# Kernel optimization log

Hardware: AMD Instinct MI355X
Metric: run time of the kernel (lower is better)

## Reference

```python
import math
import jax, jax.numpy as jnp
import numpy as np

B, N, D = 8, 1024, 1024
H, TKQ, TV = 16, 64, 64
DOUT = H * TV  # 1024, equals D
EPS = 1e-5


def _layer_norm(x, g, b):
    mu = jnp.mean(x, axis=-1, keepdims=True)
    var = jnp.mean((x - mu) ** 2, axis=-1, keepdims=True)
    return (x - mu) * jax.lax.rsqrt(var + EPS) * g + b


def setup_inputs() -> dict:
    key = jax.random.key(0)
    ks = jax.random.split(key, 16)
    s_w = 1.0 / math.sqrt(D)
    inp = {
        "tokens": jax.random.normal(ks[0], (B, N, D), jnp.float32),
        "Wq": jax.random.normal(ks[1], (H, D, TKQ), jnp.float32) * s_w,
        "bq": jax.random.uniform(ks[2], (H, 1, TKQ), jnp.float32, -s_w, s_w),
        "Wk": jax.random.normal(ks[3], (H, D, TKQ), jnp.float32) * s_w,
        "bk": jax.random.uniform(ks[4], (H, 1, TKQ), jnp.float32, -s_w, s_w),
        "Wv": jax.random.normal(ks[5], (H, D, TV), jnp.float32) * s_w,
        "bv": jax.random.uniform(ks[6], (H, 1, TV), jnp.float32, -s_w, s_w),
        "W1": jax.random.normal(ks[7], (DOUT, DOUT), jnp.float32) * (1.0 / math.sqrt(DOUT)),
        "b1": jax.random.uniform(ks[8], (DOUT,), jnp.float32, -s_w, s_w),
        "W2": jax.random.normal(ks[9], (DOUT, DOUT), jnp.float32) * (1.0 / math.sqrt(DOUT)),
        "b2": jax.random.uniform(ks[10], (DOUT,), jnp.float32, -s_w, s_w),
        "g1": jnp.ones((DOUT,), jnp.float32),
        "be1": jnp.zeros((DOUT,), jnp.float32),
        "g2": jnp.ones((DOUT,), jnp.float32),
        "be2": jnp.zeros((DOUT,), jnp.float32),
    }
    return inp


def reference(tokens, Wq, bq, Wk, bk, Wv, bv, W1, b1, W2, b2, g1, be1, g2, be2):
    # per-head projections: tokens[:,None] @ W + b  -> [B,H,N,T]
    tq = jnp.einsum("bnd,hdt->bhnt", tokens, Wq) + bq
    tk = jnp.einsum("bnd,hdt->bhnt", tokens, Wk) + bk
    tv = jnp.einsum("bnd,hdt->bhnt", tokens, Wv) + bv
    # non-standard scale: sqrt(num_heads * dim_tv)
    scale = math.sqrt(H * TV)
    scores = jnp.einsum("bhqt,bhkt->bhqk", tq, tk) / scale
    attn = jax.nn.softmax(scores, axis=-1)
    out = jnp.einsum("bhqk,bhkt->bhqt", attn, tv)  # [B,H,N,TV]
    # original flatten order: (B,N,TV,H) -> reshape(B,N,TV*H)
    out = jnp.transpose(out, (0, 2, 3, 1)).reshape(B, N, TV * H)
    # post-LN SAB path
    h = out + tokens
    h = _layer_norm(h, g1, be1)
    ff = jax.nn.relu(h @ W1 + b1) @ W2 + b2
    h = h + ff
    return _layer_norm(h, g2, be2)
```

## Files before the change

kernel.cpp:

```cpp
#include <hip/hip_runtime.h>
#include <hip/hip_bf16.h>

#define BB 8
#define NN_ 1024
#define DD 1024
#define HH 16
#define TT_ 64
#define MM (BB * NN_)

typedef __attribute__((ext_vector_type(8))) short short8;
typedef __attribute__((ext_vector_type(4))) float f32x4;
typedef __attribute__((ext_vector_type(4))) unsigned int u32x4;

__device__ __forceinline__ void g2lds16(const void* g, void* l) {
    __builtin_amdgcn_global_load_lds(
        (const __attribute__((address_space(1))) void*)g,
        (__attribute__((address_space(3))) void*)l, 16, 0, 0);
}

__device__ __forceinline__ __hip_bfloat16 f2b(float x) { return __float2bfloat16(x); }
__device__ __forceinline__ float b2f(unsigned short u) {
    unsigned v = (unsigned)u << 16;
    return __builtin_bit_cast(float, v);
}

__device__ __forceinline__ unsigned cvtpk(float a, float b) {
    unsigned r;
    asm("v_cvt_pk_bf16_f32 %0, %1, %2" : "=v"(r) : "v"(a), "v"(b));
    return r;
}

__global__ __launch_bounds__(256) void k_cvt_tokens(const float* __restrict__ in,
                                                    __hip_bfloat16* __restrict__ out) {
    int i = (blockIdx.x * 256 + threadIdx.x) * 4;
    float4 v = *(const float4*)&in[i];
    out[i + 0] = f2b(v.x); out[i + 1] = f2b(v.y);
    out[i + 2] = f2b(v.z); out[i + 3] = f2b(v.w);
}

__global__ __launch_bounds__(256) void k_cvt_wqkv(const float* __restrict__ Wq,
                                                  const float* __restrict__ Wk,
                                                  const float* __restrict__ Wv,
                                                  __hip_bfloat16* __restrict__ out) {
    __shared__ float tile[64][65];
    const int bid = blockIdx.x;
    const int proj = bid >> 8, h = (bid >> 4) & 15, dt = bid & 15;
    const float* W = proj == 0 ? Wq : (proj == 1 ? Wk : Wv);
    const float* src = W + ((size_t)h * 1024 + dt * 64) * 64;
    const int c = threadIdx.x & 63, r0 = threadIdx.x >> 6;
#pragma unroll
    for (int p = 0; p < 16; p++) {
        const int r = p * 4 + r0;
        tile[r][c] = src[(size_t)r * 64 + c];
    }
    __syncthreads();
    __hip_bfloat16* dst = out + (size_t)(proj * 1024 + h * 64) * 1024 + dt * 64;
#pragma unroll
    for (int p = 0; p < 16; p++) {
        const int r = p * 4 + r0;
        dst[(size_t)r * 1024 + c] = f2b(tile[c][r]);
    }
}

__global__ __launch_bounds__(256) void k_cvt_w(const float* __restrict__ W,
                                               __hip_bfloat16* __restrict__ out) {
    __shared__ float tile[64][65];
    const int ct = blockIdx.x & 15, dt = blockIdx.x >> 4;
    const float* src = W + (size_t)(dt * 64) * 1024 + ct * 64;
    const int c = threadIdx.x & 63, r0 = threadIdx.x >> 6;
#pragma unroll
    for (int p = 0; p < 16; p++) {
        const int r = p * 4 + r0;
        tile[r][c] = src[(size_t)r * 1024 + c];
    }
    __syncthreads();
    __hip_bfloat16* dst = out + (size_t)(ct * 64) * 1024 + dt * 64;
#pragma unroll
    for (int p = 0; p < 16; p++) {
        const int r = p * 4 + r0;
        dst[(size_t)r * 1024 + c] = f2b(tile[c][r]);
    }
}

template <int MODE>
__global__ __launch_bounds__(256) void k_gemm(
    const __hip_bfloat16* __restrict__ A, const __hip_bfloat16* __restrict__ Bt,
    const float* __restrict__ bias0, const float* __restrict__ bias1,
    const float* __restrict__ bias2,
    __hip_bfloat16* __restrict__ ob0, __hip_bfloat16* __restrict__ ob1,
    __hip_bfloat16* __restrict__ ob2,
    const __hip_bfloat16* __restrict__ res) {
    __shared__ __align__(16) __hip_bfloat16 As[128 * 64];
    __shared__ __align__(16) __hip_bfloat16 Bs[128 * 64];

    const int tid = threadIdx.x;
    const int wid = tid >> 6, lane = tid & 63;
    const int l15 = lane & 15, lhi = lane >> 4;
    const int wm = wid >> 1, wn = wid & 1;
    const int m0 = blockIdx.y * 128, n0 = blockIdx.x * 128;
    const int srow = lane >> 3, scol = (lane & 7) * 8;

    const __hip_bfloat16* gsrc;
    __hip_bfloat16* lbase;
    if (wid < 2) {
        gsrc = A + (size_t)(m0 + wid * 64 + srow) * 1024 + scol;
        lbase = As + wid * 64 * 64;
    } else {
        gsrc = Bt + (size_t)(n0 + (wid - 2) * 64 + srow) * 1024 + scol;
        lbase = Bs + (wid - 2) * 64 * 64;
    }

    f32x4 acc[4][4];
#pragma unroll
    for (int i = 0; i < 4; i++)
#pragma unroll
        for (int j = 0; j < 4; j++) acc[i][j] = (f32x4){0.f, 0.f, 0.f, 0.f};

    for (int kt = 0; kt < 16; ++kt) {
#pragma unroll
        for (int i = 0; i < 8; ++i)
            g2lds16(gsrc + kt * 64 + (size_t)i * 8 * 1024, lbase + i * 512);
        __syncthreads();
#pragma unroll
        for (int kk = 0; kk < 2; ++kk) {
            const int kb = kk * 32 + lhi * 8;
            short8 af[4], bfr[4];
#pragma unroll
            for (int mi = 0; mi < 4; mi++)
                af[mi] = *(const short8*)&As[(wm * 64 + mi * 16 + l15) * 64 + kb];
#pragma unroll
            for (int ni = 0; ni < 4; ni++)
                bfr[ni] = *(const short8*)&Bs[(wn * 64 + ni * 16 + l15) * 64 + kb];
#pragma unroll
            for (int mi = 0; mi < 4; mi++)
#pragma unroll
                for (int ni = 0; ni < 4; ni++)
                    acc[mi][ni] = __builtin_amdgcn_mfma_f32_16x16x32_bf16(
                        af[mi], bfr[ni], acc[mi][ni], 0, 0, 0);
        }
        __syncthreads();
    }

#pragma unroll
    for (int mi = 0; mi < 4; mi++) {
#pragma unroll
        for (int ni = 0; ni < 4; ni++) {
            const int col = n0 + wn * 64 + ni * 16 + l15;
#pragma unroll
            for (int r = 0; r < 4; r++) {
                const int m = m0 + wm * 64 + mi * 16 + lhi * 4 + r;
                float v = acc[mi][ni][r];
                if (MODE == 0) {
                    const int proj = col >> 10, hh = (col >> 6) & 15, t = col & 63;
                    const float* bp = proj == 0 ? bias0 : (proj == 1 ? bias1 : bias2);
                    v += bp[hh * 64 + t];
                    const int b = m >> 10, n = m & 1023;
                    if (proj == 0)
                        ob0[((size_t)(b * 16 + hh) * 1024 + n) * 64 + t] = f2b(v * 0.04508422f);
                    else if (proj == 1)
                        ob1[((size_t)(b * 16 + hh) * 1024 + n) * 64 + t] = f2b(v);
                    else
                        ob2[((size_t)(b * 16 + hh) * 64 + t) * 1024 + n] = f2b(v);
                } else if (MODE == 1) {
                    v += bias0[col];
                    ob0[(size_t)m * 1024 + col] = f2b(fmaxf(v, 0.f));
                } else {
                    v += bias0[col] + b2f(*(const unsigned short*)&res[(size_t)m * 1024 + col]);
                    ob0[(size_t)m * 1024 + col] = f2b(v);
                }
            }
        }
    }
}

__global__ __launch_bounds__(256) void k_attn(const __hip_bfloat16* __restrict__ Q,
                                              const __hip_bfloat16* __restrict__ Kg,
                                              const __hip_bfloat16* __restrict__ Vt,
                                              __hip_bfloat16* __restrict__ attn_out) {
    __shared__ __align__(16) __hip_bfloat16 Ks[2][64 * 64];
    __shared__ __align__(16) __hip_bfloat16 Vs[2][64 * 64];

    const int tid = threadIdx.x, wid = tid >> 6, lane = tid & 63;
    const int l15 = lane & 15, lhi = lane >> 4;
    const int bid = blockIdx.x;
    const int qb = bid & 7, head = (bid >> 3) & 15, b = bid >> 7;
    const int bh = b * 16 + head;
    const __hip_bfloat16* Qg = Q + ((size_t)bh * 1024 + qb * 128) * 64;
    const __hip_bfloat16* Kp = Kg + (size_t)bh * 1024 * 64;
    const __hip_bfloat16* Vp = Vt + (size_t)bh * 64 * 1024;
    const int srow = lane >> 3;
    const int scol = ((lane & 7) ^ srow) * 8;

    auto stageKV = [&](int t, int bufi) {
#pragma unroll
        for (int i = 0; i < 2; i++) {
            const int krow = (wid * 2 + i) * 8 + srow;
            const int kperm = (krow & 0x23) | ((krow & 0x0C) << 1) | ((krow & 0x10) >> 2);
            g2lds16(Kp + (size_t)(t * 64 + kperm) * 64 + scol, &Ks[bufi][(wid * 2 + i) * 512]);
            g2lds16(Vp + (size_t)krow * 1024 + t * 64 + scol, &Vs[bufi][(wid * 2 + i) * 512]);
        }
    };
    stageKV(0, 0);

    short8 qf[2][2];
#pragma unroll
    for (int g = 0; g < 2; g++)
#pragma unroll
        for (int c = 0; c < 2; c++)
            qf[g][c] = *(const short8*)&Qg[(size_t)(wid * 32 + g * 16 + l15) * 64 + c * 32 + lhi * 8];

    f32x4 o[2][4];
#pragma unroll
    for (int g = 0; g < 2; g++)
#pragma unroll
        for (int i = 0; i < 4; i++) o[g][i] = (f32x4){0.f, 0.f, 0.f, 0.f};
    f32x4 lacc[2] = {(f32x4){0.f, 0.f, 0.f, 0.f}, (f32x4){0.f, 0.f, 0.f, 0.f}};
    const short bf16_one = (short)0x3F80;
    const short8 ones = (short8){bf16_one, bf16_one, bf16_one, bf16_one,
                                 bf16_one, bf16_one, bf16_one, bf16_one};

    const int sw = l15 & 7;
    const int c0 = (lhi ^ sw) * 8;

    for (int t = 0; t < 16; ++t) {
        const int cur = t & 1;
        if (t < 15) {
            stageKV(t + 1, cur ^ 1);
            asm volatile("s_waitcnt vmcnt(4)" ::: "memory");
        } else {
            asm volatile("s_waitcnt vmcnt(0)" ::: "memory");
        }
        __builtin_amdgcn_s_barrier();
        asm volatile("" ::: "memory");

        f32x4 s[2][4];
        __builtin_amdgcn_s_setprio(1);
#pragma unroll
        for (int nt = 0; nt < 4; ++nt) {
            const int kr = (nt * 16 + l15) * 64;
            short8 k0 = *(const short8*)&Ks[cur][kr + c0];
            short8 k1 = *(const short8*)&Ks[cur][kr + (c0 ^ 32)];
#pragma unroll
            for (int g = 0; g < 2; g++) {
                f32x4 z = (f32x4){0.f, 0.f, 0.f, 0.f};
                z = __builtin_amdgcn_mfma_f32_16x16x32_bf16(k0, qf[g][0], z, 0, 0, 0);
                s[g][nt] = __builtin_amdgcn_mfma_f32_16x16x32_bf16(k1, qf[g][1], z, 0, 0, 0);
            }
        }
        __builtin_amdgcn_s_setprio(0);

#pragma unroll
        for (int g = 0; g < 2; g++)
#pragma unroll
            for (int nt = 0; nt < 4; nt++)
#pragma unroll
                for (int r = 0; r < 4; r++) s[g][nt][r] = __builtin_exp2f(s[g][nt][r]);

        short8 pf[2][2];
#pragma unroll
        for (int g = 0; g < 2; g++) {
            u32x4 w0 = (u32x4){cvtpk(s[g][0][0], s[g][0][1]), cvtpk(s[g][0][2], s[g][0][3]),
                               cvtpk(s[g][1][0], s[g][1][1]), cvtpk(s[g][1][2], s[g][1][3])};
            u32x4 w1 = (u32x4){cvtpk(s[g][2][0], s[g][2][1]), cvtpk(s[g][2][2], s[g][2][3]),
                               cvtpk(s[g][3][0], s[g][3][1]), cvtpk(s[g][3][2], s[g][3][3])};
            pf[g][0] = __builtin_bit_cast(short8, w0);
            pf[g][1] = __builtin_bit_cast(short8, w1);
        }

        __builtin_amdgcn_s_setprio(1);
#pragma unroll
        for (int g = 0; g < 2; g++) {
            lacc[g] = __builtin_amdgcn_mfma_f32_16x16x32_bf16(pf[g][0], ones, lacc[g], 0, 0, 0);
            lacc[g] = __builtin_amdgcn_mfma_f32_16x16x32_bf16(pf[g][1], ones, lacc[g], 0, 0, 0);
        }
#pragma unroll
        for (int tt = 0; tt < 4; tt++) {
            const int vr = (tt * 16 + l15) * 64;
            short8 v0 = *(const short8*)&Vs[cur][vr + c0];
            short8 v1 = *(const short8*)&Vs[cur][vr + (c0 ^ 32)];
#pragma unroll
            for (int g = 0; g < 2; g++) {
                o[g][tt] = __builtin_amdgcn_mfma_f32_16x16x32_bf16(pf[g][0], v0, o[g][tt], 0, 0, 0);
                o[g][tt] = __builtin_amdgcn_mfma_f32_16x16x32_bf16(pf[g][1], v1, o[g][tt], 0, 0, 0);
            }
        }
        __builtin_amdgcn_s_setprio(0);
        asm volatile("" ::: "memory");
        __builtin_amdgcn_s_barrier();
    }

#pragma unroll
    for (int g = 0; g < 2; g++)
#pragma unroll
        for (int r = 0; r < 4; r++) {
            const float inv_r = 1.f / lacc[g][r];
            const int row = qb * 128 + wid * 32 + g * 16 + lhi * 4 + r;
#pragma unroll
            for (int tt = 0; tt < 4; tt++) {
                const int ch = (tt * 16 + l15) * 16 + head;
                attn_out[((size_t)(b * 1024 + row)) * 1024 + ch] = f2b(o[g][tt][r] * inv_r);
            }
        }
}

__global__ __launch_bounds__(256) void k_ln1(const __hip_bfloat16* __restrict__ x1,
                                             const float* __restrict__ x2,
                                             const float* __restrict__ g,
                                             const float* __restrict__ be,
                                             __hip_bfloat16* __restrict__ y) {
    const int row = blockIdx.x;
    const int tid = threadIdx.x, wid = tid >> 6, lane = tid & 63;
    const int c = tid * 4;
    const ushort4 u = *(const ushort4*)&x1[(size_t)row * 1024 + c];
    float4 xv;
    xv.x = b2f(u.x); xv.y = b2f(u.y); xv.z = b2f(u.z); xv.w = b2f(u.w);
    float4 a = *(const float4*)&x2[(size_t)row * 1024 + c];
    xv.x += a.x; xv.y += a.y; xv.z += a.z; xv.w += a.w;
    float s = xv.x + xv.y + xv.z + xv.w;
    float q = xv.x * xv.x + xv.y * xv.y + xv.z * xv.z + xv.w * xv.w;
#pragma unroll
    for (int msk = 1; msk < 64; msk <<= 1) {
        s += __shfl_xor(s, msk);
        q += __shfl_xor(q, msk);
    }
    __shared__ float ss[4], qq[4];
    if (lane == 0) { ss[wid] = s; qq[wid] = q; }
    __syncthreads();
    s = ss[0] + ss[1] + ss[2] + ss[3];
    q = qq[0] + qq[1] + qq[2] + qq[3];
    const float mu = s * (1.f / 1024.f);
    const float var = q * (1.f / 1024.f) - mu * mu;
    const float rs = rsqrtf(var + 1e-5f);
    float4 gv = *(const float4*)&g[c];
    float4 bv = *(const float4*)&be[c];
    __hip_bfloat16* d = y + (size_t)row * 1024 + c;
    d[0] = f2b((xv.x - mu) * rs * gv.x + bv.x);
    d[1] = f2b((xv.y - mu) * rs * gv.y + bv.y);
    d[2] = f2b((xv.z - mu) * rs * gv.z + bv.z);
    d[3] = f2b((xv.w - mu) * rs * gv.w + bv.w);
}

__global__ __launch_bounds__(256) void k_ln2(const __hip_bfloat16* __restrict__ x,
                                             const float* __restrict__ g,
                                             const float* __restrict__ be,
                                             float* __restrict__ y) {
    const int row = blockIdx.x;
    const int tid = threadIdx.x, wid = tid >> 6, lane = tid & 63;
    const int c = tid * 4;
    const ushort4 u = *(const ushort4*)&x[(size_t)row * 1024 + c];
    float4 xv;
    xv.x = b2f(u.x); xv.y = b2f(u.y); xv.z = b2f(u.z); xv.w = b2f(u.w);
    float s = xv.x + xv.y + xv.z + xv.w;
    float q = xv.x * xv.x + xv.y * xv.y + xv.z * xv.z + xv.w * xv.w;
#pragma unroll
    for (int msk = 1; msk < 64; msk <<= 1) {
        s += __shfl_xor(s, msk);
        q += __shfl_xor(q, msk);
    }
    __shared__ float ss[4], qq[4];
    if (lane == 0) { ss[wid] = s; qq[wid] = q; }
    __syncthreads();
    s = ss[0] + ss[1] + ss[2] + ss[3];
    q = qq[0] + qq[1] + qq[2] + qq[3];
    const float mu = s * (1.f / 1024.f);
    const float var = q * (1.f / 1024.f) - mu * mu;
    const float rs = rsqrtf(var + 1e-5f);
    float4 gv = *(const float4*)&g[c];
    float4 bv = *(const float4*)&be[c];
    float4 yv;
    yv.x = (xv.x - mu) * rs * gv.x + bv.x;
    yv.y = (xv.y - mu) * rs * gv.y + bv.y;
    yv.z = (xv.z - mu) * rs * gv.z + bv.z;
    yv.w = (xv.w - mu) * rs * gv.w + bv.w;
    *(float4*)&y[(size_t)row * 1024 + c] = yv;
}

extern "C" void kernel_launch(void* const* d_in, const int* in_sizes, int n_in,
                              void* d_out, int out_size, void* d_ws, size_t ws_size,
                              hipStream_t stream) {
    const float* tokens = (const float*)d_in[0];
    const float* Wq  = (const float*)d_in[1];
    const float* bq  = (const float*)d_in[2];
    const float* Wk  = (const float*)d_in[3];
    const float* bk  = (const float*)d_in[4];
    const float* Wv  = (const float*)d_in[5];
    const float* bv  = (const float*)d_in[6];
    const float* W1  = (const float*)d_in[7];
    const float* b1  = (const float*)d_in[8];
    const float* W2  = (const float*)d_in[9];
    const float* b2  = (const float*)d_in[10];
    const float* g1  = (const float*)d_in[11];
    const float* be1 = (const float*)d_in[12];
    const float* g2  = (const float*)d_in[13];
    const float* be2 = (const float*)d_in[14];

    char* ws = (char*)d_ws;
    const size_t MB = 1024 * 1024;
    __hip_bfloat16* tok_b  = (__hip_bfloat16*)(ws + 0);
    __hip_bfloat16* Wqkv_t = (__hip_bfloat16*)(ws + 16 * MB);
    __hip_bfloat16* W1t    = (__hip_bfloat16*)(ws + 22 * MB);
    __hip_bfloat16* W2t    = (__hip_bfloat16*)(ws + 24 * MB);
    __hip_bfloat16* Qb     = (__hip_bfloat16*)(ws + 26 * MB);
    __hip_bfloat16* Kb     = (__hip_bfloat16*)(ws + 42 * MB);
    __hip_bfloat16* Vtb    = (__hip_bfloat16*)(ws + 58 * MB);
    __hip_bfloat16* attn_b = (__hip_bfloat16*)(ws + 74 * MB);
    __hip_bfloat16* h1     = (__hip_bfloat16*)(ws + 90 * MB);
    __hip_bfloat16* t1     = (__hip_bfloat16*)(ws + 26 * MB);
    __hip_bfloat16* h2     = (__hip_bfloat16*)(ws + 42 * MB);

    k_cvt_tokens<<<8192, 256, 0, stream>>>(tokens, tok_b);
    k_cvt_wqkv<<<768, 256, 0, stream>>>(Wq, Wk, Wv, Wqkv_t);
    k_cvt_w<<<256, 256, 0, stream>>>(W1, W1t);
    k_cvt_w<<<256, 256, 0, stream>>>(W2, W2t);

    k_gemm<0><<<dim3(24, 64), 256, 0, stream>>>(tok_b, Wqkv_t, bq, bk, bv,
                                                Qb, Kb, Vtb, nullptr);
    k_attn<<<1024, 256, 0, stream>>>(Qb, Kb, Vtb, attn_b);
    k_ln1<<<8192, 256, 0, stream>>>(attn_b, tokens, g1, be1, h1);
    k_gemm<1><<<dim3(8, 64), 256, 0, stream>>>(h1, W1t, b1, nullptr, nullptr,
                                               t1, nullptr, nullptr, nullptr);
    k_gemm<2><<<dim3(8, 64), 256, 0, stream>>>(t1, W2t, b2, nullptr, nullptr,
                                               h2, nullptr, nullptr, h1);
    k_ln2<<<8192, 256, 0, stream>>>(h2, g2, be2, (float*)d_out);
}
```

Before: 267.3 us.

## Double-buffer GEMM LDS tiles with XOR swizzle and prefetch overlap

The GEMM kernel now keeps two LDS buffers for the A and B tiles and issues the global-to-LDS loads for the next K tile before computing on the current one, using explicit vmcnt waits and raw barriers. The global source column is XOR-swizzled by row, so LDS fragment reads spread across banks instead of conflicting. s_setprio raises wave priority around the MFMA section. The goal is to hide global load latency and remove LDS bank conflicts. The cost is doubled LDS use (64KB), which may lower occupancy, and the correctness of the vmcnt accounting is delicate.

```diff
diff --git a/kernel.cpp b/kernel.cpp
--- a/kernel.cpp
+++ b/kernel.cpp
@@ -90,25 +90,30 @@
     __hip_bfloat16* __restrict__ ob0, __hip_bfloat16* __restrict__ ob1,
     __hip_bfloat16* __restrict__ ob2,
     const __hip_bfloat16* __restrict__ res) {
-    __shared__ __align__(16) __hip_bfloat16 As[128 * 64];
-    __shared__ __align__(16) __hip_bfloat16 Bs[128 * 64];
+    __shared__ __align__(16) __hip_bfloat16 As[2][128 * 64];
+    __shared__ __align__(16) __hip_bfloat16 Bs[2][128 * 64];
 
     const int tid = threadIdx.x;
     const int wid = tid >> 6, lane = tid & 63;
     const int l15 = lane & 15, lhi = lane >> 4;
     const int wm = wid >> 1, wn = wid & 1;
     const int m0 = blockIdx.y * 128, n0 = blockIdx.x * 128;
-    const int srow = lane >> 3, scol = (lane & 7) * 8;
+    const int srow = lane >> 3;
+    const int scol = ((lane & 7) ^ srow) * 8;
 
     const __hip_bfloat16* gsrc;
-    __hip_bfloat16* lbase;
-    if (wid < 2) {
+    if (wid < 2)
         gsrc = A + (size_t)(m0 + wid * 64 + srow) * 1024 + scol;
-        lbase = As + wid * 64 * 64;
-    } else {
+    else
         gsrc = Bt + (size_t)(n0 + (wid - 2) * 64 + srow) * 1024 + scol;
-        lbase = Bs + (wid - 2) * 64 * 64;
-    }
+    const int lofs = (wid & 1) * 4096;
+
+    auto stage = [&](int kt, int bufi) {
+        __hip_bfloat16* lb = (wid < 2) ? &As[bufi][lofs] : &Bs[bufi][lofs];
+#pragma unroll
+        for (int i = 0; i < 8; ++i)
+            g2lds16(gsrc + kt * 64 + (size_t)i * 8 * 1024, lb + i * 512);
+    };
 
     f32x4 acc[4][4];
 #pragma unroll
@@ -116,21 +121,30 @@
 #pragma unroll
         for (int j = 0; j < 4; j++) acc[i][j] = (f32x4){0.f, 0.f, 0.f, 0.f};
 
+    stage(0, 0);
+    const int swz = l15 & 7;
+
     for (int kt = 0; kt < 16; ++kt) {
-#pragma unroll
-        for (int i = 0; i < 8; ++i)
-            g2lds16(gsrc + kt * 64 + (size_t)i * 8 * 1024, lbase + i * 512);
-        __syncthreads();
+        const int cur = kt & 1;
+        if (kt < 15) {
+            stage(kt + 1, cur ^ 1);
+            asm volatile("s_waitcnt vmcnt(8)" ::: "memory");
+        } else {
+            asm volatile("s_waitcnt vmcnt(0)" ::: "memory");
+        }
+        __builtin_amdgcn_s_barrier();
+        asm volatile("" ::: "memory");
+        __builtin_amdgcn_s_setprio(1);
 #pragma unroll
         for (int kk = 0; kk < 2; ++kk) {
-            const int kb = kk * 32 + lhi * 8;
+            const int ch = ((kk * 4 + lhi) ^ swz) * 8;
             short8 af[4], bfr[4];
 #pragma unroll
             for (int mi = 0; mi < 4; mi++)
-                af[mi] = *(const short8*)&As[(wm * 64 + mi * 16 + l15) * 64 + kb];
+                af[mi] = *(const short8*)&As[cur][(wm * 64 + mi * 16 + l15) * 64 + ch];
 #pragma unroll
             for (int ni = 0; ni < 4; ni++)
-                bfr[ni] = *(const short8*)&Bs[(wn * 64 + ni * 16 + l15) * 64 + kb];
+                bfr[ni] = *(const short8*)&Bs[cur][(wn * 64 + ni * 16 + l15) * 64 + ch];
 #pragma unroll
             for (int mi = 0; mi < 4; mi++)
 #pragma unroll
@@ -138,7 +152,9 @@
                     acc[mi][ni] = __builtin_amdgcn_mfma_f32_16x16x32_bf16(
                         af[mi], bfr[ni], acc[mi][ni], 0, 0, 0);
         }
-        __syncthreads();
+        __builtin_amdgcn_s_setprio(0);
+        asm volatile("" ::: "memory");
+        __builtin_amdgcn_s_barrier();
     }
 
 #pragma unroll
```

New measurement: 251.2 us. 1.06x faster.
